# Performance work log

Hardware: AMD Instinct MI355X
Metric: run time of the kernel (lower is better)

The kernel has to match this reference:

```python
import jax, jax.numpy as jnp
import numpy as np

B, L, HID, NH = 2, 2048, 1024, 16
HD = HID // NH  # 64


def setup_inputs() -> dict:
    key = jax.random.key(0)
    ks = jax.random.split(key, 12)
    s = 1.0 / np.sqrt(HID)
    query = jax.random.normal(ks[0], (B, L, HID), jnp.float32)
    key_t = jax.random.normal(ks[1], (B, L, HID), jnp.float32)
    value = jax.random.normal(ks[2], (B, L, HID), jnp.float32)
    # key padding mask: True = valid token; random lengths in [1024, 2048]
    lengths = jax.random.randint(ks[3], (B,), L // 2, L + 1)
    key_mask = jnp.arange(L)[None, :] < lengths[:, None]  # [B, K] bool
    # attn_mask: True = blocked (causal upper triangle), 2D branch [Q, K]
    attn_mask = jnp.triu(jnp.ones((L, L), jnp.bool_), k=1)
    Wq = jax.random.normal(ks[4], (HID, HID), jnp.float32) * s
    Wk = jax.random.normal(ks[5], (HID, HID), jnp.float32) * s
    Wv = jax.random.normal(ks[6], (HID, HID), jnp.float32) * s
    Wo = jax.random.normal(ks[7], (HID, HID), jnp.float32) * s
    bq = jax.random.normal(ks[8], (HID,), jnp.float32) * 0.01
    bk = jax.random.normal(ks[9], (HID,), jnp.float32) * 0.01
    bv = jax.random.normal(ks[10], (HID,), jnp.float32) * 0.01
    bo = jax.random.normal(ks[11], (HID,), jnp.float32) * 0.01
    return {"query": query, "key": key_t, "value": value,
            "key_mask": key_mask, "attn_mask": attn_mask,
            "Wq": Wq, "bq": bq, "Wk": Wk, "bk": bk,
            "Wv": Wv, "bv": bv, "Wo": Wo, "bo": bo}


def reference(query, key, value, key_mask, attn_mask,
              Wq, bq, Wk, bk, Wv, bv, Wo, bo):
    Bq, Q, _ = query.shape
    K = key.shape[1]
    # projections (torch Linear: x @ W.T + b), split heads -> [B, H, L, HD]
    def proj(x, W, b, L_):
        return (x @ W.T + b).reshape(Bq, L_, NH, HD).transpose(0, 2, 1, 3)
    q = proj(query, Wq, bq, Q)
    k = proj(key, Wk, bk, K)
    v = proj(value, Wv, bv, K)
    scores = jnp.einsum('bhqd,bhkd->bhqk', q, k) / np.sqrt(HD)
    blocked = attn_mask[None, None, :, :]                 # True = blocked
    kmask = key_mask[:, None, None, :]                    # True = valid
    valid = (~blocked) & kmask                            # [B,H,Q,K] (bcast)
    scores = jnp.where(blocked, -10000.0, scores)
    scores = jnp.where(kmask, scores, -10000.0)
    weights = jax.nn.softmax(scores, axis=-1)
    weights = weights * valid.astype(weights.dtype)
    weights = weights / jnp.maximum(weights.sum(-1, keepdims=True), 1e-6)
    attended = jnp.einsum('bhqk,bhkd->bhqd', weights, v)
    attended = attended.transpose(0, 2, 1, 3).reshape(Bq, Q, HID)
    return attended @ Wo.T + bo
```

## Files before the change

kernel.cpp:

```cpp
#include <hip/hip_runtime.h>
#include <hip/hip_bf16.h>
#include <stdint.h>


#define L_SEQ 2048
#define HID 1024
#define NHEAD 16
#define HD 64

typedef __attribute__((ext_vector_type(8))) short bf16x8;
typedef __attribute__((ext_vector_type(8))) unsigned short u16x8;
typedef __attribute__((ext_vector_type(4))) float f32x4;

__device__ __forceinline__ unsigned short f2bf(float f) {
  unsigned int u = __builtin_bit_cast(unsigned int, f);
  u += 0x7fffu + ((u >> 16) & 1u);
  return (unsigned short)(u >> 16);
}

__device__ __forceinline__ unsigned int pk2bf(float a, float b) {
  unsigned int r;
  asm("v_cvt_pk_bf16_f32 %0, %1, %2" : "=v"(r) : "v"(a), "v"(b));
  return r;
}

__device__ __forceinline__ void gl_lds16(const void* g, void* l) {
  __builtin_amdgcn_global_load_lds(
      (const __attribute__((address_space(1))) unsigned int*)(uintptr_t)g,
      (__attribute__((address_space(3))) unsigned int*)(uint32_t)(uintptr_t)l,
      16, 0, 0);
}

__device__ __forceinline__ f32x4 mfma16(bf16x8 a, bf16x8 b, f32x4 c) {
  return __builtin_amdgcn_mfma_f32_16x16x32_bf16(a, b, c, 0, 0, 0);
}

__global__ __launch_bounds__(256)
void convert_all_kernel(const float* __restrict__ q, const float* __restrict__ k,
                        const float* __restrict__ v, const float* __restrict__ wq,
                        const float* __restrict__ wk, const float* __restrict__ wv,
                        const float* __restrict__ wo, const unsigned int* __restrict__ km,
                        unsigned short* __restrict__ qb, unsigned short* __restrict__ kb,
                        unsigned short* __restrict__ vb, unsigned short* __restrict__ wqb,
                        unsigned short* __restrict__ wkb, unsigned short* __restrict__ wvb,
                        unsigned short* __restrict__ wob, int* __restrict__ lens) {
  __shared__ int red[256];
  const int bid = blockIdx.x;
  const int t = threadIdx.x;
  if (bid == 8192) {
    unsigned int w0 = km[0];
    bool u8mode = (w0 != 1u);
    for (int b = 0; b < 2; ++b) {
      int cnt = 0;
      if (u8mode) {
        const unsigned char* p = (const unsigned char*)km + b * L_SEQ;
        for (int i = t; i < L_SEQ; i += 256) cnt += (p[i] != 0) ? 1 : 0;
      } else {
        const unsigned int* p = km + b * L_SEQ;
        for (int i = t; i < L_SEQ; i += 256) cnt += (p[i] != 0) ? 1 : 0;
      }
      red[t] = cnt;
      __syncthreads();
      for (int s = 128; s > 0; s >>= 1) {
        if (t < s) red[t] += red[t + s];
        __syncthreads();
      }
      if (t == 0) lens[b] = red[0];
      __syncthreads();
    }
    return;
  }
  const float* src;
  unsigned short* dst;
  int base;
  if (bid < 6144) {
    int s = bid >> 11;
    base = (bid & 2047) * 2048;
    src = s == 0 ? q : (s == 1 ? k : v);
    dst = s == 0 ? qb : (s == 1 ? kb : vb);
  } else {
    int r = bid - 6144;
    int s = r >> 9;
    base = (r & 511) * 2048;
    src = s == 0 ? wq : (s == 1 ? wk : (s == 2 ? wv : wo));
    dst = s == 0 ? wqb : (s == 1 ? wkb : (s == 2 ? wvb : wob));
  }
  int i = base + t * 8;
  float4 a = *(const float4*)(src + i);
  float4 b4 = *(const float4*)(src + i + 4);
  u16x8 o;
  o[0] = f2bf(a.x); o[1] = f2bf(a.y); o[2] = f2bf(a.z); o[3] = f2bf(a.w);
  o[4] = f2bf(b4.x); o[5] = f2bf(b4.y); o[6] = f2bf(b4.z); o[7] = f2bf(b4.w);
  *(u16x8*)(dst + i) = o;
}

__device__ __forceinline__ void gemm128_core(const unsigned short* __restrict__ A,
                                             const unsigned short* __restrict__ W,
                                             int m0, int n0, int K,
                                             unsigned short* As, unsigned short* Bs,
                                             f32x4 acc[4][4]) {
  const int tid = threadIdx.x;
  const int w = tid >> 6, lane = tid & 63;
  const int l15 = lane & 15, l4 = lane >> 4;
  const int wr = w >> 1, wc = w & 1;
#pragma unroll
  for (int i = 0; i < 4; ++i)
#pragma unroll
    for (int j = 0; j < 4; ++j) acc[i][j] = (f32x4){0.f, 0.f, 0.f, 0.f};

  for (int k0 = 0; k0 < K; k0 += 32) {
#pragma unroll
    for (int i = 0; i < 2; ++i) {
      int c = i * 256 + tid;
      int row = c >> 2, col = (c & 3) * 8;
      gl_lds16(A + (size_t)(m0 + row) * K + k0 + col, (char*)As + (i * 256 + w * 64) * 16);
      gl_lds16(W + (size_t)(n0 + row) * K + k0 + col, (char*)Bs + (i * 256 + w * 64) * 16);
    }
    __syncthreads();
    bf16x8 af[4], bfr[4];
#pragma unroll
    for (int i = 0; i < 4; ++i)
      af[i] = *(const bf16x8*)(As + (wr * 64 + i * 16 + l15) * 32 + l4 * 8);
#pragma unroll
    for (int j = 0; j < 4; ++j)
      bfr[j] = *(const bf16x8*)(Bs + (wc * 64 + j * 16 + l15) * 32 + l4 * 8);
    __builtin_amdgcn_s_setprio(1);
#pragma unroll
    for (int i = 0; i < 4; ++i)
#pragma unroll
      for (int j = 0; j < 4; ++j) acc[i][j] = mfma16(af[i], bfr[j], acc[i][j]);
    __builtin_amdgcn_s_setprio(0);
    __syncthreads();
  }
}

__global__ __launch_bounds__(256)
void qkv_gemm_kernel(const unsigned short* __restrict__ qb, const unsigned short* __restrict__ kb,
                     const unsigned short* __restrict__ vb, const unsigned short* __restrict__ wq,
                     const unsigned short* __restrict__ wk, const unsigned short* __restrict__ wv,
                     const float* __restrict__ bq, const float* __restrict__ bk,
                     const float* __restrict__ bv, unsigned short* __restrict__ Qp,
                     unsigned short* __restrict__ Kp, unsigned short* __restrict__ Vtp) {
  __shared__ unsigned short As[128 * 32];
  __shared__ unsigned short Bs[128 * 32];
  const int z = blockIdx.z;
  const unsigned short* A = z == 0 ? qb : (z == 1 ? kb : vb);
  const unsigned short* W = z == 0 ? wq : (z == 1 ? wk : wv);
  const float* bias = z == 0 ? bq : (z == 1 ? bk : bv);
  const int m0 = blockIdx.y * 128, n0 = blockIdx.x * 128;
  f32x4 acc[4][4];
  gemm128_core(A, W, m0, n0, HID, As, Bs, acc);

  const int tid = threadIdx.x;
  const int w = tid >> 6, lane = tid & 63;
  const int l15 = lane & 15, l4 = lane >> 4;
  const int wr = w >> 1, wc = w & 1;
  const float scale = (z == 0) ? 0.125f * 1.44269504089f : 1.0f;
#pragma unroll
  for (int i = 0; i < 4; ++i)
#pragma unroll
    for (int j = 0; j < 4; ++j)
#pragma unroll
      for (int r = 0; r < 4; ++r) {
        int grow = m0 + wr * 64 + i * 16 + l4 * 4 + r;
        int gcol = n0 + wc * 64 + j * 16 + l15;
        float v = (acc[i][j][r] + bias[gcol]) * scale;
        int bb = grow >> 11, ll = grow & 2047;
        int hh = gcol >> 6, d = gcol & 63;
        unsigned short o = f2bf(v);
        if (z == 0)
          Qp[((size_t)(bb * NHEAD + hh) * L_SEQ + ll) * HD + d] = o;
        else if (z == 1)
          Kp[((size_t)(bb * NHEAD + hh) * L_SEQ + ll) * HD + d] = o;
        else
          Vtp[((size_t)(bb * NHEAD + hh) * HD + d) * L_SEQ + ll] = o;
      }
}

__global__ __launch_bounds__(256)
void out_gemm_kernel(const unsigned short* __restrict__ att, const unsigned short* __restrict__ wo,
                     const float* __restrict__ bo, float* __restrict__ out) {
  __shared__ unsigned short As[128 * 32];
  __shared__ unsigned short Bs[128 * 32];
  const int m0 = blockIdx.y * 128, n0 = blockIdx.x * 128;
  f32x4 acc[4][4];
  gemm128_core(att, wo, m0, n0, HID, As, Bs, acc);

  const int tid = threadIdx.x;
  const int w = tid >> 6, lane = tid & 63;
  const int l15 = lane & 15, l4 = lane >> 4;
  const int wr = w >> 1, wc = w & 1;
#pragma unroll
  for (int i = 0; i < 4; ++i)
#pragma unroll
    for (int j = 0; j < 4; ++j)
#pragma unroll
      for (int r = 0; r < 4; ++r) {
        int grow = m0 + wr * 64 + i * 16 + l4 * 4 + r;
        int gcol = n0 + wc * 64 + j * 16 + l15;
        out[(size_t)grow * HID + gcol] = acc[i][j][r] + bo[gcol];
      }
}

__global__ __launch_bounds__(512)
void attn_kernel(const unsigned short* __restrict__ Qp, const unsigned short* __restrict__ Kp,
                 const unsigned short* __restrict__ Vtp, unsigned short* __restrict__ att,
                 const int* __restrict__ lens) {
  __shared__ unsigned short Ks[2][64 * 64];
  __shared__ unsigned short Vs[2][64 * 64];
  __shared__ unsigned short Ps[8][16 * 72];

  const int x = blockIdx.x, bh = blockIdx.y;
  const int b = bh >> 4, h = bh & 15;
  const int tid = threadIdx.x, w = tid >> 6, lane = tid & 63;
  const int l15 = lane & 15, l4 = lane >> 4;
  const int len = lens[b];
  const int sub = (w < 4) ? x : (31 - x);
  const int qw0 = sub * 64 + (w & 3) * 16;

  const unsigned short* Qg = Qp + (size_t)bh * L_SEQ * HD;
  const unsigned short* Kg = Kp + (size_t)bh * L_SEQ * HD;
  const unsigned short* Vg = Vtp + (size_t)bh * HD * L_SEQ;

  const int rr = tid >> 3, cb = tid & 7;
  const int swz = (cb ^ (rr & 7)) * 8;
  const unsigned short* KgRow = Kg + (size_t)rr * HD + swz;
  const unsigned short* VgRow = Vg + (size_t)rr * L_SEQ + swz;

  bf16x8 qf[2];
#pragma unroll
  for (int kk = 0; kk < 2; ++kk)
    qf[kk] = *(const bf16x8*)(Qg + (size_t)(qw0 + l15) * HD + kk * 32 + l4 * 8);

  f32x4 acc[4];
#pragma unroll
  for (int n = 0; n < 4; ++n) acc[n] = (f32x4){0.f, 0.f, 0.f, 0.f};
  float mq = -1e30f, lq = 0.f;

  int koff[4][2];
#pragma unroll
  for (int n = 0; n < 4; ++n)
#pragma unroll
    for (int kk = 0; kk < 2; ++kk) {
      int row = n * 16 + l15;
      koff[n][kk] = row * 128 + (((l4 + kk * 4) ^ (row & 7)) * 16);
    }

  const int len_r = ((len + 63) >> 6) << 6;
  const int hi_end = 64 * (32 - x);
  const int kv_end = (hi_end < len_r) ? hi_end : len_r;
  const int nt = kv_end >> 6;

  gl_lds16(KgRow, (char*)&Ks[0][0] + w * 1024);
  gl_lds16(VgRow, (char*)&Vs[0][0] + w * 1024);
  __syncthreads();

  int cur = 0;
  for (int t = 0; t < nt; ++t) {
    const int k0 = t * 64;
    if (t + 1 < nt) {
      const int k1 = k0 + 64;
      gl_lds16(KgRow + (size_t)k1 * HD, (char*)&Ks[cur ^ 1][0] + w * 1024);
      gl_lds16(VgRow + k1, (char*)&Vs[cur ^ 1][0] + w * 1024);
    }
    if (k0 <= qw0 + 15) {
      const char* Kb = (const char*)&Ks[cur][0];
      const char* Vb = (const char*)&Vs[cur][0];
      f32x4 s[4];
#pragma unroll
      for (int n = 0; n < 4; ++n) s[n] = (f32x4){0.f, 0.f, 0.f, 0.f};
      __builtin_amdgcn_s_setprio(1);
#pragma unroll
      for (int kk = 0; kk < 2; ++kk) {
#pragma unroll
        for (int n = 0; n < 4; ++n)
          s[n] = mfma16(*(const bf16x8*)(Kb + koff[n][kk]), qf[kk], s[n]);
      }
      __builtin_amdgcn_s_setprio(0);
      if (!(k0 + 63 <= qw0 && k0 + 64 <= len)) {
        const int qa = qw0 + l15;
#pragma unroll
        for (int n = 0; n < 4; ++n)
#pragma unroll
          for (int r = 0; r < 4; ++r) {
            int ka = k0 + n * 16 + l4 * 4 + r;
            if (ka > qa || ka >= len) s[n][r] = -1e30f;
          }
      }
      float v01 = fmaxf(fmaxf(s[0][0], s[0][1]), fmaxf(s[0][2], s[0][3]));
      float v23 = fmaxf(fmaxf(s[1][0], s[1][1]), fmaxf(s[1][2], s[1][3]));
      float v45 = fmaxf(fmaxf(s[2][0], s[2][1]), fmaxf(s[2][2], s[2][3]));
      float v67 = fmaxf(fmaxf(s[3][0], s[3][1]), fmaxf(s[3][2], s[3][3]));
      float v = fmaxf(fmaxf(v01, v23), fmaxf(v45, v67));
      v = fmaxf(v, __shfl_xor(v, 16));
      v = fmaxf(v, __shfl_xor(v, 32));
      float mold = mq;
      float mnew = fmaxf(mold, v);
      mq = mnew;
      float alpha = __builtin_amdgcn_exp2f(mold - mnew);
      float rs = 0.f;
#pragma unroll
      for (int n = 0; n < 4; ++n)
#pragma unroll
        for (int r = 0; r < 4; ++r) {
          float p = __builtin_amdgcn_exp2f(s[n][r] - mnew);
          s[n][r] = p;
          rs += p;
        }
      rs += __shfl_xor(rs, 16);
      rs += __shfl_xor(rs, 32);
      lq = lq * alpha + rs;
      float ar[4];
#pragma unroll
      for (int r = 0; r < 4; ++r) ar[r] = __shfl(alpha, l4 * 4 + r, 64);
#pragma unroll
      for (int n = 0; n < 4; ++n)
#pragma unroll
        for (int r = 0; r < 4; ++r) acc[n][r] *= ar[r];
#pragma unroll
      for (int n = 0; n < 4; ++n) {
        uint2 pw;
        pw.x = pk2bf(s[n][0], s[n][1]);
        pw.y = pk2bf(s[n][2], s[n][3]);
        *(uint2*)(&Ps[w][l15 * 72 + n * 16 + l4 * 4]) = pw;
      }
      bf16x8 pf[2];
#pragma unroll
      for (int kk = 0; kk < 2; ++kk)
        pf[kk] = *(const bf16x8*)(&Ps[w][l15 * 72 + kk * 32 + l4 * 8]);
      __builtin_amdgcn_s_setprio(1);
#pragma unroll
      for (int kk = 0; kk < 2; ++kk) {
#pragma unroll
        for (int n = 0; n < 4; ++n)
          acc[n] = mfma16(pf[kk], *(const bf16x8*)(Vb + koff[n][kk]), acc[n]);
      }
      __builtin_amdgcn_s_setprio(0);
    }
    __syncthreads();
    cur ^= 1;
  }

  float invq = 1.0f / lq;
  float invr[4];
#pragma unroll
  for (int r = 0; r < 4; ++r) invr[r] = __shfl(invq, l4 * 4 + r, 64);
#pragma unroll
  for (int r = 0; r < 4; ++r) {
    int qa = qw0 + l4 * 4 + r;
#pragma unroll
    for (int n = 0; n < 4; ++n)
      att[((size_t)(b * L_SEQ + qa)) * HID + h * HD + n * 16 + l15] = f2bf(acc[n][r] * invr[r]);
  }
}

extern "C" void kernel_launch(void* const* d_in, const int* in_sizes, int n_in,
                              void* d_out, int out_size, void* d_ws, size_t ws_size,
                              hipStream_t stream) {
  const float* query = (const float*)d_in[0];
  const float* key = (const float*)d_in[1];
  const float* value = (const float*)d_in[2];
  const unsigned int* key_mask = (const unsigned int*)d_in[3];
  const float* Wq = (const float*)d_in[5];
  const float* bq = (const float*)d_in[6];
  const float* Wk = (const float*)d_in[7];
  const float* bk = (const float*)d_in[8];
  const float* Wv = (const float*)d_in[9];
  const float* bv = (const float*)d_in[10];
  const float* Wo = (const float*)d_in[11];
  const float* bo = (const float*)d_in[12];

  char* ws = (char*)d_ws;
  const size_t SZ_X = (size_t)4096 * 1024 * 2;
  const size_t SZ_W = (size_t)1024 * 1024 * 2;
  unsigned short* qb = (unsigned short*)(ws);
  unsigned short* kb = (unsigned short*)(ws + SZ_X);
  unsigned short* vb = (unsigned short*)(ws + 2 * SZ_X);
  unsigned short* wqb = (unsigned short*)(ws + 3 * SZ_X);
  unsigned short* wkb = (unsigned short*)(ws + 3 * SZ_X + SZ_W);
  unsigned short* wvb = (unsigned short*)(ws + 3 * SZ_X + 2 * SZ_W);
  unsigned short* wob = (unsigned short*)(ws + 3 * SZ_X + 3 * SZ_W);
  unsigned short* Qp = (unsigned short*)(ws + 3 * SZ_X + 4 * SZ_W);
  unsigned short* Kp = (unsigned short*)(ws + 4 * SZ_X + 4 * SZ_W);
  unsigned short* Vtp = (unsigned short*)(ws + 5 * SZ_X + 4 * SZ_W);
  unsigned short* att = (unsigned short*)(ws + 6 * SZ_X + 4 * SZ_W);
  int* lens = (int*)(ws + 7 * SZ_X + 4 * SZ_W);

  convert_all_kernel<<<8193, 256, 0, stream>>>(query, key, value, Wq, Wk, Wv, Wo, key_mask,
                                               qb, kb, vb, wqb, wkb, wvb, wob, lens);
  qkv_gemm_kernel<<<dim3(8, 32, 3), 256, 0, stream>>>(qb, kb, vb, wqb, wkb, wvb, bq, bk, bv,
                                                      Qp, Kp, Vtp);
  attn_kernel<<<dim3(16, 32), 512, 0, stream>>>(Qp, Kp, Vtp, att, lens);
  out_gemm_kernel<<<dim3(8, 32), 256, 0, stream>>>(att, wob, bo, (float*)d_out);
}
```

Measured before the change: 146.8 us.

## Fuse activation fp32-to-bf16 conversion into QKV GEMM and double-buffer GEMM tiles

The standalone conversion of the query, key and value activations to bf16 is dropped. The QKV GEMM now loads fp32 A tiles into registers, packs them to bf16 and writes them to LDS, which removes a full write and re-read of three bf16 activation buffers. Both GEMM cores now double-buffer their LDS tiles, prefetching the next K slice while the MFMAs run. The V-transpose store is vectorized into packed uint2 writes. In exchange, the fp32 A loads are twice as wide as the old bf16 loads and go through registers, which raises register pressure, and the doubled LDS use may lower occupancy.

```diff
diff --git a/kernel.cpp b/kernel.cpp
--- a/kernel.cpp
+++ b/kernel.cpp
@@ -36,18 +36,16 @@
 }
 
 __global__ __launch_bounds__(256)
-void convert_all_kernel(const float* __restrict__ q, const float* __restrict__ k,
-                        const float* __restrict__ v, const float* __restrict__ wq,
-                        const float* __restrict__ wk, const float* __restrict__ wv,
-                        const float* __restrict__ wo, const unsigned int* __restrict__ km,
-                        unsigned short* __restrict__ qb, unsigned short* __restrict__ kb,
-                        unsigned short* __restrict__ vb, unsigned short* __restrict__ wqb,
-                        unsigned short* __restrict__ wkb, unsigned short* __restrict__ wvb,
-                        unsigned short* __restrict__ wob, int* __restrict__ lens) {
+void convert_w_kernel(const float* __restrict__ wq, const float* __restrict__ wk,
+                      const float* __restrict__ wv, const float* __restrict__ wo,
+                      const unsigned int* __restrict__ km,
+                      unsigned short* __restrict__ wqb, unsigned short* __restrict__ wkb,
+                      unsigned short* __restrict__ wvb, unsigned short* __restrict__ wob,
+                      int* __restrict__ lens) {
   __shared__ int red[256];
   const int bid = blockIdx.x;
   const int t = threadIdx.x;
-  if (bid == 8192) {
+  if (bid == 2048) {
     unsigned int w0 = km[0];
     bool u8mode = (w0 != 1u);
     for (int b = 0; b < 2; ++b) {
@@ -70,21 +68,10 @@
     }
     return;
   }
-  const float* src;
-  unsigned short* dst;
-  int base;
-  if (bid < 6144) {
-    int s = bid >> 11;
-    base = (bid & 2047) * 2048;
-    src = s == 0 ? q : (s == 1 ? k : v);
-    dst = s == 0 ? qb : (s == 1 ? kb : vb);
-  } else {
-    int r = bid - 6144;
-    int s = r >> 9;
-    base = (r & 511) * 2048;
-    src = s == 0 ? wq : (s == 1 ? wk : (s == 2 ? wv : wo));
-    dst = s == 0 ? wqb : (s == 1 ? wkb : (s == 2 ? wvb : wob));
-  }
+  int s = bid >> 9;
+  int base = (bid & 511) * 2048;
+  const float* src = s == 0 ? wq : (s == 1 ? wk : (s == 2 ? wv : wo));
+  unsigned short* dst = s == 0 ? wqb : (s == 1 ? wkb : (s == 2 ? wvb : wob));
   int i = base + t * 8;
   float4 a = *(const float4*)(src + i);
   float4 b4 = *(const float4*)(src + i + 4);
@@ -94,11 +81,11 @@
   *(u16x8*)(dst + i) = o;
 }
 
-__device__ __forceinline__ void gemm128_core(const unsigned short* __restrict__ A,
-                                             const unsigned short* __restrict__ W,
-                                             int m0, int n0, int K,
-                                             unsigned short* As, unsigned short* Bs,
-                                             f32x4 acc[4][4]) {
+__device__ __forceinline__ void gemm128_f32A_core(const float* __restrict__ A,
+                                                  const unsigned short* __restrict__ W,
+                                                  int m0, int n0, int K,
+                                                  unsigned short* As, unsigned short* Bs,
+                                                  f32x4 acc[4][4]) {
   const int tid = threadIdx.x;
   const int w = tid >> 6, lane = tid & 63;
   const int l15 = lane & 15, l4 = lane >> 4;
@@ -108,22 +95,128 @@
 #pragma unroll
     for (int j = 0; j < 4; ++j) acc[i][j] = (f32x4){0.f, 0.f, 0.f, 0.f};
 
-  for (int k0 = 0; k0 < K; k0 += 32) {
+  const int arow = tid >> 1, acolh = (tid & 1) * 16;
+  const float* Ag = A + (size_t)(m0 + arow) * K + acolh;
+  char* AsW = (char*)As + arow * 64 + acolh * 2;
+  const int nk = K >> 5;
+
+  {
+    float4 a0 = *(const float4*)(Ag);
+    float4 a1 = *(const float4*)(Ag + 4);
+    float4 a2 = *(const float4*)(Ag + 8);
+    float4 a3 = *(const float4*)(Ag + 12);
+    uint4 p0, p1;
+    p0.x = pk2bf(a0.x, a0.y); p0.y = pk2bf(a0.z, a0.w);
+    p0.z = pk2bf(a1.x, a1.y); p0.w = pk2bf(a1.z, a1.w);
+    p1.x = pk2bf(a2.x, a2.y); p1.y = pk2bf(a2.z, a2.w);
+    p1.z = pk2bf(a3.x, a3.y); p1.w = pk2bf(a3.z, a3.w);
+    *(uint4*)(AsW) = p0;
+    *(uint4*)(AsW + 16) = p1;
 #pragma unroll
     for (int i = 0; i < 2; ++i) {
       int c = i * 256 + tid;
       int row = c >> 2, col = (c & 3) * 8;
-      gl_lds16(A + (size_t)(m0 + row) * K + k0 + col, (char*)As + (i * 256 + w * 64) * 16);
-      gl_lds16(W + (size_t)(n0 + row) * K + k0 + col, (char*)Bs + (i * 256 + w * 64) * 16);
+      gl_lds16(W + (size_t)(n0 + row) * K + col, (char*)Bs + (i * 256 + w * 64) * 16);
+    }
+  }
+  __syncthreads();
+
+  int cur = 0;
+  for (int t = 0; t < nk; ++t) {
+    const int k0 = t * 32;
+    float4 a0, a1, a2, a3;
+    const bool more = (t + 1 < nk);
+    if (more) {
+      const float* Agn = Ag + k0 + 32;
+      a0 = *(const float4*)(Agn);
+      a1 = *(const float4*)(Agn + 4);
+      a2 = *(const float4*)(Agn + 8);
+      a3 = *(const float4*)(Agn + 12);
+#pragma unroll
+      for (int i = 0; i < 2; ++i) {
+        int c = i * 256 + tid;
+        int row = c >> 2, col = (c & 3) * 8;
+        gl_lds16(W + (size_t)(n0 + row) * K + k0 + 32 + col,
+                 (char*)Bs + (cur ^ 1) * 8192 + (i * 256 + w * 64) * 16);
+      }
+    }
+    const unsigned short* Asb = As + cur * 4096;
+    const unsigned short* Bsb = Bs + cur * 4096;
+    bf16x8 af[4], bfr[4];
+#pragma unroll
+    for (int i = 0; i < 4; ++i)
+      af[i] = *(const bf16x8*)(Asb + (wr * 64 + i * 16 + l15) * 32 + l4 * 8);
+#pragma unroll
+    for (int j = 0; j < 4; ++j)
+      bfr[j] = *(const bf16x8*)(Bsb + (wc * 64 + j * 16 + l15) * 32 + l4 * 8);
+    __builtin_amdgcn_s_setprio(1);
+#pragma unroll
+    for (int i = 0; i < 4; ++i)
+#pragma unroll
+      for (int j = 0; j < 4; ++j) acc[i][j] = mfma16(af[i], bfr[j], acc[i][j]);
+    __builtin_amdgcn_s_setprio(0);
+    if (more) {
+      uint4 p0, p1;
+      p0.x = pk2bf(a0.x, a0.y); p0.y = pk2bf(a0.z, a0.w);
+      p0.z = pk2bf(a1.x, a1.y); p0.w = pk2bf(a1.z, a1.w);
+      p1.x = pk2bf(a2.x, a2.y); p1.y = pk2bf(a2.z, a2.w);
+      p1.z = pk2bf(a3.x, a3.y); p1.w = pk2bf(a3.z, a3.w);
+      char* dst = AsW + (cur ^ 1) * 8192;
+      *(uint4*)(dst) = p0;
+      *(uint4*)(dst + 16) = p1;
     }
     __syncthreads();
+    cur ^= 1;
+  }
+}
+
+__device__ __forceinline__ void gemm128_bf_core(const unsigned short* __restrict__ A,
+                                                const unsigned short* __restrict__ W,
+                                                int m0, int n0, int K,
+                                                unsigned short* As, unsigned short* Bs,
+                                                f32x4 acc[4][4]) {
+  const int tid = threadIdx.x;
+  const int w = tid >> 6, lane = tid & 63;
+  const int l15 = lane & 15, l4 = lane >> 4;
+  const int wr = w >> 1, wc = w & 1;
+#pragma unroll
+  for (int i = 0; i < 4; ++i)
+#pragma unroll
+    for (int j = 0; j < 4; ++j) acc[i][j] = (f32x4){0.f, 0.f, 0.f, 0.f};
+
+  const int nk = K >> 5;
+#pragma unroll
+  for (int i = 0; i < 2; ++i) {
+    int c = i * 256 + tid;
+    int row = c >> 2, col = (c & 3) * 8;
+    gl_lds16(A + (size_t)(m0 + row) * K + col, (char*)As + (i * 256 + w * 64) * 16);
+    gl_lds16(W + (size_t)(n0 + row) * K + col, (char*)Bs + (i * 256 + w * 64) * 16);
+  }
+  __syncthreads();
+
+  int cur = 0;
+  for (int t = 0; t < nk; ++t) {
+    const int k0 = t * 32;
+    if (t + 1 < nk) {
+#pragma unroll
+      for (int i = 0; i < 2; ++i) {
+        int c = i * 256 + tid;
+        int row = c >> 2, col = (c & 3) * 8;
+        gl_lds16(A + (size_t)(m0 + row) * K + k0 + 32 + col,
+                 (char*)As + (cur ^ 1) * 8192 + (i * 256 + w * 64) * 16);
+        gl_lds16(W + (size_t)(n0 + row) * K + k0 + 32 + col,
+                 (char*)Bs + (cur ^ 1) * 8192 + (i * 256 + w * 64) * 16);
+      }
+    }
+    const unsigned short* Asb = As + cur * 4096;
+    const unsigned short* Bsb = Bs + cur * 4096;
     bf16x8 af[4], bfr[4];
 #pragma unroll
     for (int i = 0; i < 4; ++i)
-      af[i] = *(const bf16x8*)(As + (wr * 64 + i * 16 + l15) * 32 + l4 * 8);
+      af[i] = *(const bf16x8*)(Asb + (wr * 64 + i * 16 + l15) * 32 + l4 * 8);
 #pragma unroll
     for (int j = 0; j < 4; ++j)
-      bfr[j] = *(const bf16x8*)(Bs + (wc * 64 + j * 16 + l15) * 32 + l4 * 8);
+      bfr[j] = *(const bf16x8*)(Bsb + (wc * 64 + j * 16 + l15) * 32 + l4 * 8);
     __builtin_amdgcn_s_setprio(1);
 #pragma unroll
     for (int i = 0; i < 4; ++i)
@@ -131,60 +224,73 @@
       for (int j = 0; j < 4; ++j) acc[i][j] = mfma16(af[i], bfr[j], acc[i][j]);
     __builtin_amdgcn_s_setprio(0);
     __syncthreads();
+    cur ^= 1;
   }
 }
 
 __global__ __launch_bounds__(256)
-void qkv_gemm_kernel(const unsigned short* __restrict__ qb, const unsigned short* __restrict__ kb,
-                     const unsigned short* __restrict__ vb, const unsigned short* __restrict__ wq,
+void qkv_gemm_kernel(const float* __restrict__ qf32, const float* __restrict__ kf32,
+                     const float* __restrict__ vf32, const unsigned short* __restrict__ wq,
                      const unsigned short* __restrict__ wk, const unsigned short* __restrict__ wv,
                      const float* __restrict__ bq, const float* __restrict__ bk,
                      const float* __restrict__ bv, unsigned short* __restrict__ Qp,
                      unsigned short* __restrict__ Kp, unsigned short* __restrict__ Vtp) {
-  __shared__ unsigned short As[128 * 32];
-  __shared__ unsigned short Bs[128 * 32];
+  __shared__ unsigned short As[2 * 128 * 32];
+  __shared__ unsigned short Bs[2 * 128 * 32];
   const int z = blockIdx.z;
-  const unsigned short* A = z == 0 ? qb : (z == 1 ? kb : vb);
+  const float* A = z == 0 ? qf32 : (z == 1 ? kf32 : vf32);
   const unsigned short* W = z == 0 ? wq : (z == 1 ? wk : wv);
   const float* bias = z == 0 ? bq : (z == 1 ? bk : bv);
   const int m0 = blockIdx.y * 128, n0 = blockIdx.x * 128;
   f32x4 acc[4][4];
-  gemm128_core(A, W, m0, n0, HID, As, Bs, acc);
+  gemm128_f32A_core(A, W, m0, n0, HID, As, Bs, acc);
 
   const int tid = threadIdx.x;
   const int w = tid >> 6, lane = tid & 63;
   const int l15 = lane & 15, l4 = lane >> 4;
   const int wr = w >> 1, wc = w & 1;
   const float scale = (z == 0) ? 0.125f * 1.44269504089f : 1.0f;
-#pragma unroll
-  for (int i = 0; i < 4; ++i)
-#pragma unroll
-    for (int j = 0; j < 4; ++j)
-#pragma unroll
-      for (int r = 0; r < 4; ++r) {
-        int grow = m0 + wr * 64 + i * 16 + l4 * 4 + r;
+  if (z == 2) {
+#pragma unroll
+    for (int i = 0; i < 4; ++i)
+#pragma unroll
+      for (int j = 0; j < 4; ++j) {
+        int grow0 = m0 + wr * 64 + i * 16 + l4 * 4;
         int gcol = n0 + wc * 64 + j * 16 + l15;
-        float v = (acc[i][j][r] + bias[gcol]) * scale;
-        int bb = grow >> 11, ll = grow & 2047;
+        float bv_ = bias[gcol];
+        int bb = grow0 >> 11, ll0 = grow0 & 2047;
         int hh = gcol >> 6, d = gcol & 63;
-        unsigned short o = f2bf(v);
-        if (z == 0)
-          Qp[((size_t)(bb * NHEAD + hh) * L_SEQ + ll) * HD + d] = o;
-        else if (z == 1)
-          Kp[((size_t)(bb * NHEAD + hh) * L_SEQ + ll) * HD + d] = o;
-        else
-          Vtp[((size_t)(bb * NHEAD + hh) * HD + d) * L_SEQ + ll] = o;
-      }
+        uint2 pw;
+        pw.x = pk2bf(acc[i][j][0] + bv_, acc[i][j][1] + bv_);
+        pw.y = pk2bf(acc[i][j][2] + bv_, acc[i][j][3] + bv_);
+        *(uint2*)(&Vtp[((size_t)(bb * NHEAD + hh) * HD + d) * L_SEQ + ll0]) = pw;
+      }
+  } else {
+    unsigned short* P = (z == 0) ? Qp : Kp;
+#pragma unroll
+    for (int i = 0; i < 4; ++i)
+#pragma unroll
+      for (int j = 0; j < 4; ++j)
+#pragma unroll
+        for (int r = 0; r < 4; ++r) {
+          int grow = m0 + wr * 64 + i * 16 + l4 * 4 + r;
+          int gcol = n0 + wc * 64 + j * 16 + l15;
+          float v = (acc[i][j][r] + bias[gcol]) * scale;
+          int bb = grow >> 11, ll = grow & 2047;
+          int hh = gcol >> 6, d = gcol & 63;
+          P[((size_t)(bb * NHEAD + hh) * L_SEQ + ll) * HD + d] = f2bf(v);
+        }
+  }
 }
 
 __global__ __launch_bounds__(256)
 void out_gemm_kernel(const unsigned short* __restrict__ att, const unsigned short* __restrict__ wo,
                      const float* __restrict__ bo, float* __restrict__ out) {
-  __shared__ unsigned short As[128 * 32];
-  __shared__ unsigned short Bs[128 * 32];
+  __shared__ unsigned short As[2 * 128 * 32];
+  __shared__ unsigned short Bs[2 * 128 * 32];
   const int m0 = blockIdx.y * 128, n0 = blockIdx.x * 128;
   f32x4 acc[4][4];
-  gemm128_core(att, wo, m0, n0, HID, As, Bs, acc);
+  gemm128_bf_core(att, wo, m0, n0, HID, As, Bs, acc);
 
   const int tid = threadIdx.x;
   const int w = tid >> 6, lane = tid & 63;
@@ -373,9 +479,6 @@
   char* ws = (char*)d_ws;
   const size_t SZ_X = (size_t)4096 * 1024 * 2;
   const size_t SZ_W = (size_t)1024 * 1024 * 2;
-  unsigned short* qb = (unsigned short*)(ws);
-  unsigned short* kb = (unsigned short*)(ws + SZ_X);
-  unsigned short* vb = (unsigned short*)(ws + 2 * SZ_X);
   unsigned short* wqb = (unsigned short*)(ws + 3 * SZ_X);
   unsigned short* wkb = (unsigned short*)(ws + 3 * SZ_X + SZ_W);
   unsigned short* wvb = (unsigned short*)(ws + 3 * SZ_X + 2 * SZ_W);
@@ -386,10 +489,10 @@
   unsigned short* att = (unsigned short*)(ws + 6 * SZ_X + 4 * SZ_W);
   int* lens = (int*)(ws + 7 * SZ_X + 4 * SZ_W);
 
-  convert_all_kernel<<<8193, 256, 0, stream>>>(query, key, value, Wq, Wk, Wv, Wo, key_mask,
-                                               qb, kb, vb, wqb, wkb, wvb, wob, lens);
-  qkv_gemm_kernel<<<dim3(8, 32, 3), 256, 0, stream>>>(qb, kb, vb, wqb, wkb, wvb, bq, bk, bv,
-                                                      Qp, Kp, Vtp);
+  convert_w_kernel<<<2049, 256, 0, stream>>>(Wq, Wk, Wv, Wo, key_mask,
+                                             wqb, wkb, wvb, wob, lens);
+  qkv_gemm_kernel<<<dim3(8, 32, 3), 256, 0, stream>>>(query, key, value, wqb, wkb, wvb,
+                                                      bq, bk, bv, Qp, Kp, Vtp);
   attn_kernel<<<dim3(16, 32), 512, 0, stream>>>(Qp, Kp, Vtp, att, lens);
   out_gemm_kernel<<<dim3(8, 32), 256, 0, stream>>>(att, wob, bo, (float*)d_out);
 }
```

New measurement: 145.4 us. About the same (-0.9%).
